# Optimization experiments

Hardware: AMD Instinct MI355X
Metric: run time of the kernel (lower is better)

The kernel has to match this reference:

```python
import jax, jax.numpy as jnp
import numpy as np

NUM_CLASSES = 20
MEM_SIZE = 512      # memory_bank_size
MAX_VIEWS = 512
TEMP = 0.1
MOMENTUM = 0.999
IGNORE_IDX = 255
AUX_IDX = 254
EPS = 1e-12


def _nearest_resize(gt, Ho, Wo):
    # torch F.interpolate(mode='nearest'): src = floor(dst * in/out)
    B, Hi, Wi = gt.shape
    ri = (jnp.arange(Ho) * Hi) // Ho
    ci = (jnp.arange(Wo) * Wi) // Wo
    return gt[:, ri][:, :, ci]


def _norm_flat(p):
    # L2-normalize over channels, then [B, C, H, W] -> [B, H*W, C]
    p = p / jnp.maximum(jnp.linalg.norm(p, axis=1, keepdims=True), EPS)
    B, C = p.shape[0], p.shape[1]
    return p.reshape(B, C, -1).transpose(0, 2, 1)


def setup_inputs() -> dict:
    key = jax.random.key(0)
    k1, k2, k3, k4, k5 = jax.random.split(key, 5)
    B, D, H, W = 4, 256, 128, 128
    Hg, Wg = 512, 512
    return {
        'main_proj': jax.random.normal(k1, (B, D, H, W), dtype=jnp.float32),
        'main_gt': jax.random.randint(k2, (B, Hg, Wg), 0, NUM_CLASSES).astype(jnp.int64),
        'aux_proj': jax.random.normal(k3, (B, D, H, W), dtype=jnp.float32),
        'aux_gt': jax.random.randint(k4, (B, Hg, Wg), 0, NUM_CLASSES).astype(jnp.int64),
        'memory_bank': jax.random.normal(k5, (NUM_CLASSES, MEM_SIZE, D), dtype=jnp.float32),
    }


def reference(main_proj, main_gt, aux_proj, aux_gt, memory_bank):
    C, M, D = memory_bank.shape
    B, _, H, W = main_proj.shape
    mg = _nearest_resize(main_gt, H, W)
    ag = _nearest_resize(aux_gt, aux_proj.shape[2], aux_proj.shape[3])

    embd = jnp.concatenate([_norm_flat(main_proj), _norm_flat(aux_proj)], axis=1)
    embd = embd.reshape(-1, D)                       # [N, D]
    label = jnp.concatenate([mg.reshape(B, -1), ag.reshape(B, -1)], axis=1).reshape(-1)

    valid = label != IGNORE_IDX
    label = jnp.where(label == AUX_IDX, C - 1, label)

    # per-class gather: stable argsort puts class-c pixels first (deterministic
    # stand-in for torch.randperm selection)
    masks = (label[None, :] == jnp.arange(C)[:, None]) & valid[None, :]   # [C, N]
    counts = masks.sum(axis=1)                                           # [C]
    order = jnp.argsort(~masks, axis=1, stable=True)[:, :M]              # [C, M]
    sel = embd[order]                                                    # [C, M, D]
    sel_valid = jnp.arange(M)[None, :] < counts[:, None]                 # [C, M]

    # momentum scatter-update to memory bank (no grad through features)
    upd = MOMENTUM * memory_bank + (1.0 - MOMENTUM) * jax.lax.stop_gradient(sel)
    upd = upd / jnp.maximum(jnp.linalg.norm(upd, axis=2, keepdims=True), EPS)
    bank = jnp.where(sel_valid[..., None], upd, memory_bank)             # [C, M, D]

    # anchors from current batch (with grad)
    V = min(MAX_VIEWS, M)
    anchors = sel[:, :V].reshape(C * V, D)
    a_valid = sel_valid[:, :V].reshape(-1)
    a_lbl = jnp.repeat(jnp.arange(C), V)

    # contrastive samples from updated bank (constant w.r.t. grad)
    contras = bank.reshape(C * M, D)
    c_valid = jnp.linalg.norm(bank, axis=2).reshape(-1) > 0
    c_lbl = jnp.repeat(jnp.arange(C), M)

    # InfoNCE with masked softmax over valid contrastive columns
    scores = (anchors @ contras.T) / TEMP                                # [A, K]
    scores = jnp.where(c_valid[None, :], scores, -1e9)
    logp = jax.nn.log_softmax(scores, axis=1)
    pos = ((a_lbl[:, None] == c_lbl[None, :]) & c_valid[None, :]).astype(scores.dtype)
    pos_sum = (pos * logp).sum(axis=1)
    pos_cnt = pos.sum(axis=1)
    va = (pos_cnt > 0) & a_valid
    mlpp = jnp.where(va, pos_sum / jnp.maximum(pos_cnt, 1.0), 0.0)
    loss = -mlpp.sum() / jnp.maximum(va.sum(), 1).astype(scores.dtype)
    return loss
```

## Files before the change

kernel.cpp:

```cpp
#include <hip/hip_runtime.h>
#include <cstdint>
#include <math.h>

#define NCLS  20
#define MSZ   512
#define DIM   256
#define HW    16384
#define NPIX  131072
#define AROWS 10240
#define TEMP_INV 10.0f
#define EXP2K 14.4269504088896f

typedef __attribute__((ext_vector_type(8))) short bf16x8;
typedef __attribute__((ext_vector_type(4))) float f32x4;

__device__ __forceinline__ short f2bf(float f) {
    unsigned u = __float_as_uint(f);
    unsigned r = (u + 0x7FFFu + ((u >> 16) & 1u)) >> 16;
    return (short)r;
}
__device__ __forceinline__ float bf2f(short s) {
    return __uint_as_float(((unsigned)(unsigned short)s) << 16);
}
__device__ __forceinline__ float fexp2(float x) {
    float r;
    asm volatile("v_exp_f32 %0, %1" : "=v"(r) : "v"(x));
    return r;
}
__device__ __forceinline__ void gld16(const void* g, void* l) {
    __builtin_amdgcn_global_load_lds(
        (const __attribute__((address_space(1))) unsigned int*)(uintptr_t)g,
        (__attribute__((address_space(3))) unsigned int*)(unsigned int)(uintptr_t)l,
        16, 0, 0);
}

#define ZREG_FLOATS 15488

__global__ __launch_bounds__(256) void k_hist(const int* __restrict__ mg,
                                              const int* __restrict__ ag,
                                              int* __restrict__ labels,
                                              int* __restrict__ hist,
                                              int* __restrict__ pix2row,
                                              float* __restrict__ zreg) {
    int chunk = blockIdx.x, t = threadIdx.x;
    int lane = t & 63;
    int gi = chunk * 256 + t;
    if (gi < ZREG_FLOATS) zreg[gi] = 0.0f;

    int n = gi;
    int b = n >> 15, r = n & 32767;
    const int* g = (r < HW) ? mg : ag;
    int p = (r < HW) ? r : (r - HW);
    int h = p >> 7, w = p & 127;
    int lab = g[(((size_t)b * 512) + (size_t)(h << 2)) * 512 + (size_t)(w << 2)];
    if (lab == 255) lab = -1;
    else if (lab == 254) lab = NCLS - 1;
    labels[n] = lab;
    pix2row[n] = -1;

    __shared__ int cnt20[NCLS];
    if (t < NCLS) cnt20[t] = 0;
    __syncthreads();
#pragma unroll
    for (int c = 0; c < NCLS; ++c) {
        unsigned long long m = __ballot(lab == c);
        if (lane == 0 && m) atomicAdd(&cnt20[c], __popcll(m));
    }
    __syncthreads();
    if (t < NCLS) hist[t * 512 + chunk] = cnt20[t];
}

__global__ __launch_bounds__(256) void k_write(const int* __restrict__ labels,
                                               const int* __restrict__ hist,
                                               int* __restrict__ pix2row,
                                               int* __restrict__ counts) {
    int chunk = blockIdx.x, t = threadIdx.x;
    int lane = t & 63, wv = t >> 6;
    __shared__ int cbase[NCLS];
    __shared__ int wcnt2[4][NCLS];

#pragma unroll
    for (int cc = 0; cc < 5; ++cc) {
        int c = wv * 5 + cc;
        int s = 0;
        for (int j = lane; j < chunk; j += 64) s += hist[c * 512 + j];
#pragma unroll
        for (int o = 32; o > 0; o >>= 1) s += __shfl_down(s, o, 64);
        if (lane == 0) cbase[c] = s;
    }

    int n = chunk * 256 + t;
    int lab = labels[n];
    int myrank = 0;
#pragma unroll
    for (int c = 0; c < NCLS; ++c) {
        unsigned long long m = __ballot(lab == c);
        if (lane == 0) wcnt2[wv][c] = __popcll(m);
        if (lab == c) myrank = __popcll(m & ((1ull << lane) - 1ull));
    }
    __syncthreads();
    if (lab >= 0) {
        int base = cbase[lab] + myrank;
        for (int w = 0; w < wv; ++w) base += wcnt2[w][lab];
        if (base < MSZ) pix2row[n] = lab * MSZ + base;
    }
    if (chunk == 511 && t < NCLS)
        counts[t] = cbase[t] + wcnt2[0][t] + wcnt2[1][t] + wcnt2[2][t] + wcnt2[3][t];
}

__global__ __launch_bounds__(256) void k_scatter(const float* __restrict__ mainp,
                                                 const float* __restrict__ auxp,
                                                 const int* __restrict__ pix2row,
                                                 float* __restrict__ xF) {
    int idx = blockIdx.x * 256 + threadIdx.x;
    int p4 = idx & 4095;
    int ch = (idx >> 12) & 255;
    int bs = idx >> 20;
    int b = bs >> 1, src = bs & 1;
    const float* base = (src ? auxp : mainp) + (size_t)b * DIM * HW + (size_t)ch * HW;
    float4 v = *(const float4*)(base + p4 * 4);
    int4 pr = *(const int4*)(pix2row + bs * HW + p4 * 4);
    if (pr.x >= 0) xF[(size_t)pr.x * DIM + ch] = v.x;
    if (pr.y >= 0) xF[(size_t)pr.y * DIM + ch] = v.y;
    if (pr.z >= 0) xF[(size_t)pr.z * DIM + ch] = v.z;
    if (pr.w >= 0) xF[(size_t)pr.w * DIM + ch] = v.w;
}

__global__ __launch_bounds__(256) void k_nbc(const float* __restrict__ xF,
                                             const float* __restrict__ bank,
                                             const int* __restrict__ counts,
                                             short* __restrict__ anchorsB,
                                             short* __restrict__ contrasB,
                                             int* __restrict__ c_valid,
                                             float* __restrict__ S,
                                             int* __restrict__ pcnt) {
    int blk = blockIdx.x;
    int c = blk >> 3;
    int t = threadIdx.x, lane = t & 63, wv = t >> 6;
    int cc = counts[c];
    int base = blk * 64;
    float sacc[4] = {0.f, 0.f, 0.f, 0.f};
    int vcnt = 0;

    for (int it = 0; it < 16; ++it) {
        int a = base + it * 4 + wv;
        int m = a & 511;
        float4 xv = *(const float4*)&xF[(size_t)a * DIM + lane * 4];
        float x[4] = {xv.x, xv.y, xv.z, xv.w};
        float ss = x[0]*x[0] + x[1]*x[1] + x[2]*x[2] + x[3]*x[3];
#pragma unroll
        for (int o = 1; o < 64; o <<= 1) ss += __shfl_xor(ss, o, 64);
        float scale = 1.0f / fmaxf(sqrtf(ss), 1e-12f);
        float ax[4];
#pragma unroll
        for (int q = 0; q < 4; ++q) ax[q] = x[q] * scale;
        short4 oa;
        oa.x = f2bf(ax[0]); oa.y = f2bf(ax[1]); oa.z = f2bf(ax[2]); oa.w = f2bf(ax[3]);
        *(short4*)&anchorsB[(size_t)a * DIM + lane * 4] = oa;

        bool upd = m < cc;
        float4 bv = *(const float4*)&bank[(size_t)a * DIM + lane * 4];
        float u[4];
        u[0] = upd ? 0.999f * bv.x + 0.001f * ax[0] : bv.x;
        u[1] = upd ? 0.999f * bv.y + 0.001f * ax[1] : bv.y;
        u[2] = upd ? 0.999f * bv.z + 0.001f * ax[2] : bv.z;
        u[3] = upd ? 0.999f * bv.w + 0.001f * ax[3] : bv.w;
        float ss2 = u[0]*u[0] + u[1]*u[1] + u[2]*u[2] + u[3]*u[3];
#pragma unroll
        for (int o = 1; o < 64; o <<= 1) ss2 += __shfl_xor(ss2, o, 64);
        float nrm = sqrtf(ss2);
        float inv = 1.0f / fmaxf(nrm, 1e-12f);
        short oc[4];
        oc[0] = f2bf(upd ? u[0] * inv : bv.x);
        oc[1] = f2bf(upd ? u[1] * inv : bv.y);
        oc[2] = f2bf(upd ? u[2] * inv : bv.z);
        oc[3] = f2bf(upd ? u[3] * inv : bv.w);
        *(short4*)&contrasB[(size_t)a * DIM + lane * 4] = *(short4*)oc;
        bool valid = nrm > 0.0f;
        if (lane == 0) {
            c_valid[a] = valid ? 1 : 0;
            vcnt += valid ? 1 : 0;
        }
        if (valid) {
#pragma unroll
            for (int q = 0; q < 4; ++q) sacc[q] += bf2f(oc[q]);
        }
    }

    __shared__ float s4[4][DIM];
    __shared__ int pv[4];
#pragma unroll
    for (int q = 0; q < 4; ++q) s4[wv][lane * 4 + q] = sacc[q];
    if (lane == 0) pv[wv] = vcnt;
    __syncthreads();
    float s = s4[0][t] + s4[1][t] + s4[2][t] + s4[3][t];
    atomicAdd(&S[c * DIM + t], s);
    if (t == 0) atomicAdd(&pcnt[c], pv[0] + pv[1] + pv[2] + pv[3]);
}

__global__ __launch_bounds__(512, 4) void k_score(const short* __restrict__ A,
                                                  const short* __restrict__ Bc,
                                                  const int* __restrict__ c_valid,
                                                  float* __restrict__ row_sumexp) {
    __shared__ short As[128 * 64];
    __shared__ short Bs[256 * 64];
    const int t = threadIdx.x;
    const int lane = t & 63, wv = t >> 6;
    const int wr = wv & 1, wc = wv >> 1;
    const int qr = lane >> 4, qc = lane & 15;
    const int s7 = qc & 7;
    const int row0 = blockIdx.x * 128, col0 = blockIdx.y * 256;

    const int rl8 = t >> 3;
    const int sdat = (t & 7) ^ (rl8 & 7);
    const short* Ag = A  + (size_t)row0 * DIM;
    const short* Bg = Bc + (size_t)col0 * DIM;

    const int sl0 = ((0 + qr) ^ s7) * 8;
    const int sl1 = ((4 + qr) ^ s7) * 8;

    f32x4 acc[4][4] = {};

    auto stage = [&](int kt) {
#pragma unroll
        for (int r = 0; r < 2; ++r)
            gld16(Ag + (size_t)(r * 64 + rl8) * DIM + kt * 64 + sdat * 8,
                  &As[(r * 64 + wv * 8) * 64]);
#pragma unroll
        for (int r = 0; r < 4; ++r)
            gld16(Bg + (size_t)(r * 64 + rl8) * DIM + kt * 64 + sdat * 8,
                  &Bs[(r * 64 + wv * 8) * 64]);
    };

    stage(0);
    for (int kt = 0; kt < 4; ++kt) {
        asm volatile("s_waitcnt vmcnt(0)" ::: "memory");
        asm volatile("s_barrier" ::: "memory");

        bf16x8 a0[4], b0[4], a1[4], b1[4];
#pragma unroll
        for (int rt = 0; rt < 4; ++rt)
            a0[rt] = *(const bf16x8*)&As[(wr * 64 + rt * 16 + qc) * 64 + sl0];
#pragma unroll
        for (int ct = 0; ct < 4; ++ct)
            b0[ct] = *(const bf16x8*)&Bs[(wc * 64 + ct * 16 + qc) * 64 + sl0];
#pragma unroll
        for (int rt = 0; rt < 4; ++rt)
#pragma unroll
            for (int ct = 0; ct < 4; ++ct)
                acc[rt][ct] = __builtin_amdgcn_mfma_f32_16x16x32_bf16(a0[rt], b0[ct], acc[rt][ct], 0, 0, 0);
#pragma unroll
        for (int rt = 0; rt < 4; ++rt)
            a1[rt] = *(const bf16x8*)&As[(wr * 64 + rt * 16 + qc) * 64 + sl1];
#pragma unroll
        for (int ct = 0; ct < 4; ++ct)
            b1[ct] = *(const bf16x8*)&Bs[(wc * 64 + ct * 16 + qc) * 64 + sl1];

        asm volatile("s_waitcnt lgkmcnt(0)" ::: "memory");
        __builtin_amdgcn_sched_barrier(0);
        asm volatile("s_barrier" ::: "memory");
        if (kt < 3) stage(kt + 1);

#pragma unroll
        for (int rt = 0; rt < 4; ++rt)
#pragma unroll
            for (int ct = 0; ct < 4; ++ct)
                acc[rt][ct] = __builtin_amdgcn_mfma_f32_16x16x32_bf16(a1[rt], b1[ct], acc[rt][ct], 0, 0, 0);
    }

    float cm[4];
#pragma unroll
    for (int ct = 0; ct < 4; ++ct)
        cm[ct] = c_valid[col0 + wc * 64 + ct * 16 + qc] ? 1.0f : 0.0f;
#pragma unroll
    for (int rt = 0; rt < 4; ++rt)
#pragma unroll
        for (int r = 0; r < 4; ++r) {
            float e = cm[0] * fexp2(acc[rt][0][r] * EXP2K)
                    + cm[1] * fexp2(acc[rt][1][r] * EXP2K)
                    + cm[2] * fexp2(acc[rt][2][r] * EXP2K)
                    + cm[3] * fexp2(acc[rt][3][r] * EXP2K);
#pragma unroll
            for (int o = 1; o < 16; o <<= 1) e += __shfl_xor(e, o, 64);
            if (qc == 0)
                atomicAdd(&row_sumexp[row0 + wr * 64 + rt * 16 + qr * 4 + r], e);
        }
}

__global__ __launch_bounds__(256) void k_fin(const short* __restrict__ anchorsB,
                                             const float* __restrict__ S,
                                             const int* __restrict__ counts,
                                             const int* __restrict__ pcnt,
                                             const float* __restrict__ row_sumexp,
                                             float* __restrict__ facc,
                                             int* __restrict__ done_cnt,
                                             float* __restrict__ out) {
    int blk = blockIdx.x;
    int c = blk >> 3;
    int t = threadIdx.x, lane = t & 63, wv = t >> 6;
    int pc = pcnt[c], cc = counts[c];
    float lsum = 0.0f, vc = 0.0f;

    for (int it = 0; it < 16; ++it) {
        int a = blk * 64 + it * 4 + wv;
        short4 a4 = *(const short4*)&anchorsB[(size_t)a * DIM + lane * 4];
        float4 s4 = *(const float4*)&S[c * DIM + lane * 4];
        float dot = bf2f(a4.x) * s4.x + bf2f(a4.y) * s4.y
                  + bf2f(a4.z) * s4.z + bf2f(a4.w) * s4.w;
#pragma unroll
        for (int o = 1; o < 64; o <<= 1) dot += __shfl_xor(dot, o, 64);
        if (lane == 0 && (a & 511) < cc && pc > 0) {
            float lse = logf(row_sumexp[a]);
            lsum += (TEMP_INV * dot - (float)pc * lse) / (float)pc;
            vc += 1.0f;
        }
    }

    __shared__ float wls[4], wvc[4];
    if (lane == 0) { wls[wv] = lsum; wvc[wv] = vc; }
    __syncthreads();
    if (t == 0) {
        atomicAdd(&facc[0], wls[0] + wls[1] + wls[2] + wls[3]);
        atomicAdd(&facc[1], wvc[0] + wvc[1] + wvc[2] + wvc[3]);
        __threadfence();
        unsigned d = atomicAdd((unsigned*)done_cnt, 1u);
        if (d == 159u) {
            __threadfence();
            float L = atomicAdd(&facc[0], 0.0f);
            float V = atomicAdd(&facc[1], 0.0f);
            out[0] = -L / fmaxf(V, 1.0f);
        }
    }
}

extern "C" void kernel_launch(void* const* d_in, const int* in_sizes, int n_in,
                              void* d_out, int out_size, void* d_ws, size_t ws_size,
                              hipStream_t stream) {
    const float* main_proj = (const float*)d_in[0];
    const int*   main_gt   = (const int*)d_in[1];
    const float* aux_proj  = (const float*)d_in[2];
    const int*   aux_gt    = (const int*)d_in[3];
    const float* bank      = (const float*)d_in[4];
    float* out = (float*)d_out;

    char* ws = (char*)d_ws;
    int*   labels     = (int*)ws;
    int*   hist       = (int*)(ws + 524288);
    int*   pix2row    = (int*)(ws + 565248);
    int*   c_valid    = (int*)(ws + 1089536);
    float* zreg       = (float*)(ws + 1130496);
    float* row_sumexp = zreg;
    float* S          = zreg + 10240;
    int*   pcnt       = (int*)(zreg + 15360);
    float* facc       = zreg + 15380;
    int*   done_cnt   = (int*)(zreg + 15382);
    int*   counts     = (int*)(ws + 1192448);
    float* xF         = (float*)(ws + 1192704);
    short* anchorsB   = (short*)(ws + 11678464);
    short* contrasB   = (short*)(ws + 16921344);

    k_hist<<<512, 256, 0, stream>>>(main_gt, aux_gt, labels, hist, pix2row, zreg);
    k_write<<<512, 256, 0, stream>>>(labels, hist, pix2row, counts);
    k_scatter<<<32768, 256, 0, stream>>>(main_proj, aux_proj, pix2row, xF);
    k_nbc<<<AROWS / 64, 256, 0, stream>>>(xF, bank, counts, anchorsB, contrasB,
                                          c_valid, S, pcnt);
    dim3 grid(AROWS / 128, AROWS / 256);
    k_score<<<grid, 512, 0, stream>>>(anchorsB, contrasB, c_valid, row_sumexp);
    k_fin<<<AROWS / 64, 256, 0, stream>>>(anchorsB, S, counts, pcnt, row_sumexp,
                                          facc, done_cnt, out);
}
```

Before: 297.8 us.

## Double-buffer score GEMM LDS tiles with K=32 steps and skip empty scatter quads

The score kernel now uses two LDS buffers of K=32 slices and prefetches the next slice right after the barrier, so global loads overlap the MFMA work and one barrier per iteration is removed. The XOR swizzle is dropped in favor of a plain row-major 32-wide layout, which may bring back LDS bank conflicts. The loop runs eight unrolled iterations instead of four. Separately, the scatter kernel loads pix2row first and returns early when all four pixels are unselected, skipping the feature read for those quads.

```diff
diff --git a/kernel.cpp b/kernel.cpp
--- a/kernel.cpp
+++ b/kernel.cpp
@@ -117,9 +117,10 @@
     int ch = (idx >> 12) & 255;
     int bs = idx >> 20;
     int b = bs >> 1, src = bs & 1;
+    int4 pr = *(const int4*)(pix2row + bs * HW + p4 * 4);
+    if ((pr.x & pr.y & pr.z & pr.w) < 0) return;
     const float* base = (src ? auxp : mainp) + (size_t)b * DIM * HW + (size_t)ch * HW;
     float4 v = *(const float4*)(base + p4 * 4);
-    int4 pr = *(const int4*)(pix2row + bs * HW + p4 * 4);
     if (pr.x >= 0) xF[(size_t)pr.x * DIM + ch] = v.x;
     if (pr.y >= 0) xF[(size_t)pr.y * DIM + ch] = v.y;
     if (pr.z >= 0) xF[(size_t)pr.z * DIM + ch] = v.z;
@@ -202,70 +203,52 @@
                                                   const short* __restrict__ Bc,
                                                   const int* __restrict__ c_valid,
                                                   float* __restrict__ row_sumexp) {
-    __shared__ short As[128 * 64];
-    __shared__ short Bs[256 * 64];
+    __shared__ short As[2][128 * 32];
+    __shared__ short Bs[2][256 * 32];
     const int t = threadIdx.x;
     const int lane = t & 63, wv = t >> 6;
     const int wr = wv & 1, wc = wv >> 1;
     const int qr = lane >> 4, qc = lane & 15;
-    const int s7 = qc & 7;
     const int row0 = blockIdx.x * 128, col0 = blockIdx.y * 256;
 
-    const int rl8 = t >> 3;
-    const int sdat = (t & 7) ^ (rl8 & 7);
+    const int rsub = lane >> 2;
+    const int ksub = (lane & 3) * 8;
     const short* Ag = A  + (size_t)row0 * DIM;
     const short* Bg = Bc + (size_t)col0 * DIM;
 
-    const int sl0 = ((0 + qr) ^ s7) * 8;
-    const int sl1 = ((4 + qr) ^ s7) * 8;
-
     f32x4 acc[4][4] = {};
 
-    auto stage = [&](int kt) {
-#pragma unroll
-        for (int r = 0; r < 2; ++r)
-            gld16(Ag + (size_t)(r * 64 + rl8) * DIM + kt * 64 + sdat * 8,
-                  &As[(r * 64 + wv * 8) * 64]);
-#pragma unroll
-        for (int r = 0; r < 4; ++r)
-            gld16(Bg + (size_t)(r * 64 + rl8) * DIM + kt * 64 + sdat * 8,
-                  &Bs[(r * 64 + wv * 8) * 64]);
+    auto stage = [&](int buf, int kt) {
+        gld16(Ag + (size_t)(wv * 16 + rsub) * DIM + kt * 32 + ksub,
+              &As[buf][(wv * 16) * 32]);
+        gld16(Bg + (size_t)(wv * 32 + rsub) * DIM + kt * 32 + ksub,
+              &Bs[buf][(wv * 32) * 32]);
+        gld16(Bg + (size_t)(wv * 32 + 16 + rsub) * DIM + kt * 32 + ksub,
+              &Bs[buf][(wv * 32 + 16) * 32]);
     };
 
-    stage(0);
-    for (int kt = 0; kt < 4; ++kt) {
+    stage(0, 0);
+#pragma unroll
+    for (int kt = 0; kt < 8; ++kt) {
+        const int buf = kt & 1;
         asm volatile("s_waitcnt vmcnt(0)" ::: "memory");
         asm volatile("s_barrier" ::: "memory");
-
-        bf16x8 a0[4], b0[4], a1[4], b1[4];
+        if (kt < 7) stage(buf ^ 1, kt + 1);
+
+        bf16x8 a[4], b[4];
 #pragma unroll
         for (int rt = 0; rt < 4; ++rt)
-            a0[rt] = *(const bf16x8*)&As[(wr * 64 + rt * 16 + qc) * 64 + sl0];
+            a[rt] = *(const bf16x8*)&As[buf][(wr * 64 + rt * 16 + qc) * 32 + qr * 8];
 #pragma unroll
         for (int ct = 0; ct < 4; ++ct)
-            b0[ct] = *(const bf16x8*)&Bs[(wc * 64 + ct * 16 + qc) * 64 + sl0];
-#pragma unroll
-        for (int rt = 0; rt < 4; ++rt)
-#pragma unroll
-            for (int ct = 0; ct < 4; ++ct)
-                acc[rt][ct] = __builtin_amdgcn_mfma_f32_16x16x32_bf16(a0[rt], b0[ct], acc[rt][ct], 0, 0, 0);
-#pragma unroll
-        for (int rt = 0; rt < 4; ++rt)
-            a1[rt] = *(const bf16x8*)&As[(wr * 64 + rt * 16 + qc) * 64 + sl1];
-#pragma unroll
-        for (int ct = 0; ct < 4; ++ct)
-            b1[ct] = *(const bf16x8*)&Bs[(wc * 64 + ct * 16 + qc) * 64 + sl1];
-
+            b[ct] = *(const bf16x8*)&Bs[buf][(wc * 64 + ct * 16 + qc) * 32 + qr * 8];
         asm volatile("s_waitcnt lgkmcnt(0)" ::: "memory");
         __builtin_amdgcn_sched_barrier(0);
-        asm volatile("s_barrier" ::: "memory");
-        if (kt < 3) stage(kt + 1);
-
 #pragma unroll
         for (int rt = 0; rt < 4; ++rt)
 #pragma unroll
             for (int ct = 0; ct < 4; ++ct)
-                acc[rt][ct] = __builtin_amdgcn_mfma_f32_16x16x32_bf16(a1[rt], b1[ct], acc[rt][ct], 0, 0, 0);
+                acc[rt][ct] = __builtin_amdgcn_mfma_f32_16x16x32_bf16(a[rt], b[ct], acc[rt][ct], 0, 0, 0);
     }
 
     float cm[4];
```

New measurement: 282.5 us. -5.1%, faster.
